# Kernel optimization log

Measured on AMD Instinct MI355X. Metric: run time of the kernel, lower is better.

The kernel has to match this reference:

```python
import jax, jax.numpy as jnp
import numpy as np

N_NODES = 50000

def gcn_conv(x, src, dst, ew, W, b):
    # PyG GCNConv: transform first, then D^-1/2 (A+I) D^-1/2 aggregation.
    h = x @ W                                   # [N, F_out]
    deg = jnp.zeros((N_NODES,), x.dtype).at[dst].add(ew)
    dis = jnp.where(deg > 0, jax.lax.rsqrt(deg), 0.0)
    norm = dis[src] * ew * dis[dst]             # [E]
    msg = norm[:, None] * h[src]                # [E, F_out]
    out = jax.ops.segment_sum(msg, dst, num_segments=N_NODES)
    return out + b

def setup_inputs() -> dict:
    key = jax.random.key(0)
    ks = jax.random.split(key, 9)
    x = jax.random.normal(ks[0], (N_NODES, 512), jnp.float32)
    edge_index = jax.random.randint(ks[1], (2, 800000), 0, N_NODES, jnp.int64)
    edge_attr = jax.random.uniform(ks[2], (800000,), jnp.float32)
    s = lambda f: 1.0 / np.sqrt(f)
    W1 = jax.random.normal(ks[3], (512, 64), jnp.float32) * s(512)
    b1 = jnp.zeros((64,), jnp.float32)
    W2 = jax.random.normal(ks[4], (64, 64), jnp.float32) * s(64)
    b2 = jnp.zeros((64,), jnp.float32)
    W3 = jax.random.normal(ks[5], (128, 128), jnp.float32) * s(128)
    b3 = jnp.zeros((128,), jnp.float32)
    return {"x": x, "edge_index": edge_index, "edge_attr": edge_attr,
            "W1": W1, "b1": b1, "W2": W2, "b2": b2, "W3": W3, "b3": b3}

def reference(x, edge_index, edge_attr, W1, b1, W2, b2, W3, b3):
    # add self-loops with weight 1 (GCNConv default)
    loops = jnp.arange(N_NODES, dtype=edge_index.dtype)
    src = jnp.concatenate([edge_index[0], loops])
    dst = jnp.concatenate([edge_index[1], loops])
    ew = jnp.concatenate([edge_attr, jnp.ones((N_NODES,), edge_attr.dtype)])
    h1 = gcn_conv(x, src, dst, ew, W1, b1)          # dropout is identity at eval
    h2 = gcn_conv(h1, src, dst, ew, W2, b2)
    h3 = gcn_conv(jnp.concatenate([h1, h2], axis=-1), src, dst, ew, W3, b3)
    return jax.nn.softmax(h3, axis=-1)
```

## Files before the change

### kernel.cpp

```cpp
#include <hip/hip_runtime.h>
#include <cstdint>
#include <cstddef>

#define NN 50000

typedef __attribute__((ext_vector_type(8))) short short8;
typedef __attribute__((ext_vector_type(4))) float f32x4;

__device__ inline ushort bf16_rne(float x) {
  uint u = __float_as_uint(x);
  uint r = u + 0x7FFFu + ((u >> 16) & 1u);
  return (ushort)(r >> 16);
}
__device__ inline float bf16_to_f(ushort h) { return __uint_as_float(((uint)h) << 16); }


#define NB2 256

__global__ __launch_bounds__(256) void k_hist(const int* __restrict__ dst,
                                              ushort* __restrict__ histmat, int E) {
  __shared__ uint lcnt[NN / 2];
  for (int i = threadIdx.x; i < NN / 2; i += 256) lcnt[i] = 0;
  __syncthreads();
  const int b = blockIdx.x;
  const int e0 = (int)((long long)E * b / NB2);
  const int e1 = (int)((long long)E * (b + 1) / NB2);
  for (int e = e0 + threadIdx.x; e < e1; e += 256) {
    int d = dst[e];
    atomicAdd(&lcnt[d >> 1], 1u << ((d & 1) * 16));
  }
  __syncthreads();
  uint* out = (uint*)(histmat + (size_t)b * NN);
  for (int i = threadIdx.x; i < NN / 2; i += 256) out[i] = lcnt[i];
}

__global__ __launch_bounds__(256) void k_colscan(ushort* __restrict__ histmat,
                                                 int* __restrict__ cnt, int N) {
  int n = blockIdx.x * 256 + threadIdx.x;
  if (n >= N) return;
  int run = 0;
  ushort* p = histmat + n;
#pragma unroll 8
  for (int b = 0; b < NB2; ++b) {
    int t = p[(size_t)b * NN];
    p[(size_t)b * NN] = (ushort)run;
    run += t;
  }
  cnt[n] = run;
}

__global__ __launch_bounds__(256) void k_scatter(const int* __restrict__ src,
                                                 const int* __restrict__ dst,
                                                 const float* __restrict__ ew,
                                                 const int* __restrict__ row_ptr,
                                                 const ushort* __restrict__ histmat,
                                                 int2* __restrict__ edge_s, int E) {
  __shared__ uint lcur[NN / 2];
  for (int i = threadIdx.x; i < NN / 2; i += 256) lcur[i] = 0;
  __syncthreads();
  const int b = blockIdx.x;
  const ushort* hb = histmat + (size_t)b * NN;
  const int e0 = (int)((long long)E * b / NB2);
  const int e1 = (int)((long long)E * (b + 1) / NB2);
  for (int e = e0 + threadIdx.x; e < e1; e += 256) {
    int d = dst[e];
    int sh = (d & 1) * 16;
    uint old = atomicAdd(&lcur[d >> 1], 1u << sh);
    int c = (int)((old >> sh) & 0xffffu);
    int pos = row_ptr[d] + (int)hb[d] + c;
    edge_s[pos] = make_int2(src[e], __float_as_int(ew[e]));
  }
}

__global__ __launch_bounds__(256) void k_degsum(const int* __restrict__ row_ptr,
                                                const int2* __restrict__ edge_s,
                                                float* __restrict__ dis, int N) {
  int n = blockIdx.x * 256 + threadIdx.x;
  if (n >= N) return;
  float sum = 1.0f;
  int e1 = row_ptr[n + 1];
  for (int p = row_ptr[n]; p < e1; ++p) sum += __int_as_float(edge_s[p].y);
  dis[n] = rsqrtf(sum);
}

__global__ __launch_bounds__(256) void k_wfix(int2* __restrict__ edge_s,
                                              const float* __restrict__ dis, int E) {
  int p = blockIdx.x * 256 + threadIdx.x;
  if (p >= E) return;
  int2 v = edge_s[p];
  edge_s[p] = make_int2(v.x, __float_as_int(dis[v.x] * __int_as_float(v.y)));
}


__global__ __launch_bounds__(256) void k_scan1(const int* __restrict__ in,
                                               int* __restrict__ out,
                                               int* __restrict__ bsum, int n) {
  __shared__ int ts[256];
  int base = blockIdx.x * 1024 + threadIdx.x * 4;
  int v[4] = {0, 0, 0, 0};
#pragma unroll
  for (int j = 0; j < 4; ++j) { int i = base + j; if (i < n) v[j] = in[i]; }
  int s = v[0] + v[1] + v[2] + v[3];
  ts[threadIdx.x] = s;
  __syncthreads();
  for (int o = 1; o < 256; o <<= 1) {
    int t = (threadIdx.x >= o) ? ts[threadIdx.x - o] : 0;
    __syncthreads();
    ts[threadIdx.x] += t;
    __syncthreads();
  }
  int run = ts[threadIdx.x] - s;
#pragma unroll
  for (int j = 0; j < 4; ++j) { int i = base + j; if (i < n) out[i] = run; run += v[j]; }
  if (threadIdx.x == 255) bsum[blockIdx.x] = ts[255];
}

__global__ void k_scan2(int* __restrict__ bsum, int nb, int* __restrict__ rpN, int E) {
  if (threadIdx.x == 0) {
    int run = 0;
    for (int b = 0; b < nb; ++b) { int t = bsum[b]; bsum[b] = run; run += t; }
    *rpN = E;
  }
}

__global__ __launch_bounds__(256) void k_scan3(int* __restrict__ out,
                                               const int* __restrict__ bsum, int n) {
  int i = blockIdx.x * 256 + threadIdx.x;
  if (i < n) out[i] += bsum[i >> 10];
}


__global__ __launch_bounds__(256) void k_wsplit(const float* __restrict__ W, int logF,
                                                int K, ushort* __restrict__ th,
                                                ushort* __restrict__ tl, int total) {
  int idx = blockIdx.x * 256 + threadIdx.x;
  if (idx >= total) return;
  int k = idx >> logF;
  int n = idx & ((1 << logF) - 1);
  float w = W[idx];
  ushort h = bf16_rne(w);
  float lof = w - bf16_to_f(h);
  ushort l = bf16_rne(lof);
  th[(size_t)n * K + k] = h;
  tl[(size_t)n * K + k] = l;
}

__global__ __launch_bounds__(256) void k_wprep(const float* __restrict__ W2,
                                               const float* __restrict__ W3,
                                               const float* __restrict__ b2,
                                               ushort* __restrict__ wch,
                                               ushort* __restrict__ wcl,
                                               float* __restrict__ bc) {
  int idx = blockIdx.x * 256 + threadIdx.x;
  int k = idx >> 7, n = idx & 127;
  float v;
  if (k < 64) {
    v = W3[k * 128 + n];
  } else {
    v = 0.f;
    const float* w2r = W2 + (k - 64) * 64;
    for (int j = 0; j < 64; ++j) v += w2r[j] * W3[(64 + j) * 128 + n];
  }
  ushort h = bf16_rne(v);
  wch[(size_t)n * 128 + k] = h;
  wcl[(size_t)n * 128 + k] = bf16_rne(v - bf16_to_f(h));
  if (idx < 128) {
    float s = 0.f;
    for (int j = 0; j < 64; ++j) s += b2[j] * W3[(64 + j) * 128 + idx];
    bc[idx] = s;
  }
}


template <int BN>
__global__ __launch_bounds__(256) void k_gemm_mfma(const float* __restrict__ A, int lda,
                                                   const ushort* __restrict__ BTh,
                                                   const ushort* __restrict__ BTl,
                                                   float* __restrict__ C, int ldc,
                                                   int N, int K) {
  constexpr int WN = BN / 2;
  constexpr int NT = WN / 16;
  __shared__ __align__(16) ushort Ah[64 * 64];
  __shared__ __align__(16) ushort Al[64 * 64];
  __shared__ __align__(16) ushort Bh[BN * 64];
  __shared__ __align__(16) ushort Bl[BN * 64];

  const int tid = threadIdx.x;
  const int lane = tid & 63;
  const int wid = tid >> 6;
  const int wm = wid >> 1;
  const int wn = wid & 1;
  const int bm = blockIdx.x * 64;
  const int l15 = lane & 15;
  const int kgrp = (lane >> 4) << 4;

  f32x4 acc[2][NT] = {};

  for (int kt = 0; kt < K; kt += 64) {
#pragma unroll
    for (int p = 0; p < 4; ++p) {
      int s = tid + p * 256;
      int m = s >> 4;
      int k4 = (s & 15) << 2;
      int gr = bm + m;
      float4 v = make_float4(0.f, 0.f, 0.f, 0.f);
      if (gr < N) v = *(const float4*)(A + (size_t)gr * lda + kt + k4);
      ushort4 h, l;
      h.x = bf16_rne(v.x); l.x = bf16_rne(v.x - bf16_to_f(h.x));
      h.y = bf16_rne(v.y); l.y = bf16_rne(v.y - bf16_to_f(h.y));
      h.z = bf16_rne(v.z); l.z = bf16_rne(v.z - bf16_to_f(h.z));
      h.w = bf16_rne(v.w); l.w = bf16_rne(v.w - bf16_to_f(h.w));
      int byo = (m * 128 + (k4 << 1)) ^ ((m & 7) << 4);
      *(ushort4*)((char*)Ah + byo) = h;
      *(ushort4*)((char*)Al + byo) = l;
    }
#pragma unroll
    for (int it = 0; it < BN / 32; ++it) {
      int s = tid + it * 256;
      int n = s >> 3;
      int kc = (s & 7) << 3;
      float4 vh = *(const float4*)(BTh + (size_t)n * K + kt + kc);
      float4 vl = *(const float4*)(BTl + (size_t)n * K + kt + kc);
      int byo = (n * 128 + (kc << 1)) ^ ((n & 7) << 4);
      *(float4*)((char*)Bh + byo) = vh;
      *(float4*)((char*)Bl + byo) = vl;
    }
    __syncthreads();
#pragma unroll
    for (int ks = 0; ks < 2; ++ks) {
      int kb = ks * 64 + kgrp;
      short8 ah[2], al[2];
#pragma unroll
      for (int i = 0; i < 2; ++i) {
        int row = wm * 32 + i * 16 + l15;
        int off = (row * 128 + kb) ^ ((row & 7) << 4);
        ah[i] = *(const short8*)((const char*)Ah + off);
        al[i] = *(const short8*)((const char*)Al + off);
      }
#pragma unroll
      for (int j = 0; j < NT; ++j) {
        int nr = wn * WN + j * 16 + l15;
        int off = (nr * 128 + kb) ^ ((nr & 7) << 4);
        short8 bh = *(const short8*)((const char*)Bh + off);
        short8 bl = *(const short8*)((const char*)Bl + off);
#pragma unroll
        for (int i = 0; i < 2; ++i) {
          acc[i][j] = __builtin_amdgcn_mfma_f32_16x16x32_bf16(ah[i], bh, acc[i][j], 0, 0, 0);
          acc[i][j] = __builtin_amdgcn_mfma_f32_16x16x32_bf16(ah[i], bl, acc[i][j], 0, 0, 0);
          acc[i][j] = __builtin_amdgcn_mfma_f32_16x16x32_bf16(al[i], bh, acc[i][j], 0, 0, 0);
        }
      }
    }
    __syncthreads();
  }

  const int r4 = (lane >> 4) << 2;
#pragma unroll
  for (int i = 0; i < 2; ++i) {
    int rowb = bm + wm * 32 + i * 16 + r4;
#pragma unroll
    for (int j = 0; j < NT; ++j) {
      int col = wn * WN + j * 16 + l15;
#pragma unroll
      for (int q = 0; q < 4; ++q) {
        int row = rowb + q;
        if (row < N) C[(size_t)row * ldc + col] = acc[i][j][q];
      }
    }
  }
}


__global__ __launch_bounds__(256) void k_gemm_smax(const float* __restrict__ A1,
                                                   const float* __restrict__ A2,
                                                   const ushort* __restrict__ BTh,
                                                   const ushort* __restrict__ BTl,
                                                   float* __restrict__ Cout,
                                                   const float* __restrict__ c,
                                                   const float* __restrict__ bc,
                                                   const float* __restrict__ b3,
                                                   int N) {
  constexpr int WN = 64, NT = 4, K = 128;
  __shared__ __align__(16) ushort smem[24576];
  ushort* Ah = smem;
  ushort* Al = smem + 4096;
  ushort* Bh = smem + 8192;
  ushort* Bl = smem + 16384;

  const int tid = threadIdx.x;
  const int lane = tid & 63;
  const int wid = tid >> 6;
  const int wm = wid >> 1;
  const int wn = wid & 1;
  const int bm = blockIdx.x * 64;
  const int l15 = lane & 15;
  const int kgrp = (lane >> 4) << 4;

  f32x4 acc[2][NT] = {};

  for (int kt = 0; kt < K; kt += 64) {
    const float* Asrc = (kt == 0) ? A1 : A2;
#pragma unroll
    for (int p = 0; p < 4; ++p) {
      int s = tid + p * 256;
      int m = s >> 4;
      int k4 = (s & 15) << 2;
      int gr = bm + m;
      float4 v = make_float4(0.f, 0.f, 0.f, 0.f);
      if (gr < N) v = *(const float4*)(Asrc + (size_t)gr * 64 + k4);
      ushort4 h, l;
      h.x = bf16_rne(v.x); l.x = bf16_rne(v.x - bf16_to_f(h.x));
      h.y = bf16_rne(v.y); l.y = bf16_rne(v.y - bf16_to_f(h.y));
      h.z = bf16_rne(v.z); l.z = bf16_rne(v.z - bf16_to_f(h.z));
      h.w = bf16_rne(v.w); l.w = bf16_rne(v.w - bf16_to_f(h.w));
      int byo = (m * 128 + (k4 << 1)) ^ ((m & 7) << 4);
      *(ushort4*)((char*)Ah + byo) = h;
      *(ushort4*)((char*)Al + byo) = l;
    }
#pragma unroll
    for (int it = 0; it < 4; ++it) {
      int s = tid + it * 256;
      int n = s >> 3;
      int kc = (s & 7) << 3;
      float4 vh = *(const float4*)(BTh + (size_t)n * K + kt + kc);
      float4 vl = *(const float4*)(BTl + (size_t)n * K + kt + kc);
      int byo = (n * 128 + (kc << 1)) ^ ((n & 7) << 4);
      *(float4*)((char*)Bh + byo) = vh;
      *(float4*)((char*)Bl + byo) = vl;
    }
    __syncthreads();
#pragma unroll
    for (int ks = 0; ks < 2; ++ks) {
      int kb = ks * 64 + kgrp;
      short8 ah[2], al[2];
#pragma unroll
      for (int i = 0; i < 2; ++i) {
        int row = wm * 32 + i * 16 + l15;
        int off = (row * 128 + kb) ^ ((row & 7) << 4);
        ah[i] = *(const short8*)((const char*)Ah + off);
        al[i] = *(const short8*)((const char*)Al + off);
      }
#pragma unroll
      for (int j = 0; j < NT; ++j) {
        int nr = wn * WN + j * 16 + l15;
        int off = (nr * 128 + kb) ^ ((nr & 7) << 4);
        short8 bh = *(const short8*)((const char*)Bh + off);
        short8 bl = *(const short8*)((const char*)Bl + off);
#pragma unroll
        for (int i = 0; i < 2; ++i) {
          acc[i][j] = __builtin_amdgcn_mfma_f32_16x16x32_bf16(ah[i], bh, acc[i][j], 0, 0, 0);
          acc[i][j] = __builtin_amdgcn_mfma_f32_16x16x32_bf16(ah[i], bl, acc[i][j], 0, 0, 0);
          acc[i][j] = __builtin_amdgcn_mfma_f32_16x16x32_bf16(al[i], bh, acc[i][j], 0, 0, 0);
        }
      }
    }
    __syncthreads();
  }

  float* hs = (float*)smem;
  float* pm = hs + 64 * 129;
  float* ps = pm + 256;

  const int r4 = (lane >> 4) << 2;
#pragma unroll
  for (int i = 0; i < 2; ++i) {
#pragma unroll
    for (int j = 0; j < NT; ++j) {
      int colb = wn * WN + j * 16 + l15;
      float cbv = bc[colb];
      float b3v = b3[colb];
#pragma unroll
      for (int q = 0; q < 4; ++q) {
        int rl = wm * 32 + i * 16 + r4 + q;
        int grow = bm + rl;
        float cv = (grow < N) ? c[grow] : 0.f;
        hs[rl * 129 + colb] = acc[i][j][q] + cv * cbv + b3v;
      }
    }
  }
  __syncthreads();

  int row = tid >> 2;
  int cs = (tid & 3) * 32;
  float ev[32];
  float m = -3.4e38f;
#pragma unroll
  for (int k = 0; k < 32; ++k) { ev[k] = hs[row * 129 + cs + k]; m = fmaxf(m, ev[k]); }
  float s = 0.f;
#pragma unroll
  for (int k = 0; k < 32; ++k) { ev[k] = __expf(ev[k] - m); s += ev[k]; }
  pm[row * 4 + (tid & 3)] = m;
  ps[row * 4 + (tid & 3)] = s;
  __syncthreads();
  float m0 = pm[row * 4 + 0], m1 = pm[row * 4 + 1];
  float m2 = pm[row * 4 + 2], m3 = pm[row * 4 + 3];
  float M = fmaxf(fmaxf(m0, m1), fmaxf(m2, m3));
  float S = ps[row * 4 + 0] * __expf(m0 - M) + ps[row * 4 + 1] * __expf(m1 - M) +
            ps[row * 4 + 2] * __expf(m2 - M) + ps[row * 4 + 3] * __expf(m3 - M);
  float f = __expf(pm[row * 4 + (tid & 3)] - M) / S;
  int grow = bm + row;
  if (grow < N) {
    float4* op = (float4*)(Cout + (size_t)grow * 128 + cs);
#pragma unroll
    for (int k = 0; k < 32; k += 4)
      op[k >> 2] = make_float4(ev[k] * f, ev[k + 1] * f, ev[k + 2] * f, ev[k + 3] * f);
  }
}


template <int LOGF, bool CSUM>
__global__ __launch_bounds__(256) void k_gather8(const float* __restrict__ t, int ldt,
                                                 const int* __restrict__ row_ptr,
                                                 const int2* __restrict__ edge_s,
                                                 const float* __restrict__ dis,
                                                 const float* __restrict__ bias,
                                                 float* __restrict__ out, int ldo,
                                                 float* __restrict__ cvec, int N) {
  constexpr int F = 1 << LOGF;
  constexpr int TPN = F / 4;
  int node = blockIdx.x * (256 / TPN) + threadIdx.x / TPN;
  if (node >= N) return;
  int f4 = (threadIdx.x % TPN) * 4;

  float4 a0, a1, a2, a3;
  a0.x = a0.y = a0.z = a0.w = 0.f;
  a1.x = a1.y = a1.z = a1.w = 0.f;
  a2.x = a2.y = a2.z = a2.w = 0.f;
  a3.x = a3.y = a3.z = a3.w = 0.f;
  float sw = 0.f;

  const int beg = row_ptr[node], end = row_ptr[node + 1];
  int i = beg;
  for (; i + 8 <= end; i += 8) {
    int2 e0 = edge_s[i], e1 = edge_s[i + 1], e2 = edge_s[i + 2], e3 = edge_s[i + 3];
    int2 e4 = edge_s[i + 4], e5 = edge_s[i + 5], e6 = edge_s[i + 6], e7 = edge_s[i + 7];
    float4 v0 = *(const float4*)(t + (size_t)e0.x * ldt + f4);
    float4 v1 = *(const float4*)(t + (size_t)e1.x * ldt + f4);
    float4 v2 = *(const float4*)(t + (size_t)e2.x * ldt + f4);
    float4 v3 = *(const float4*)(t + (size_t)e3.x * ldt + f4);
    float4 v4 = *(const float4*)(t + (size_t)e4.x * ldt + f4);
    float4 v5 = *(const float4*)(t + (size_t)e5.x * ldt + f4);
    float4 v6 = *(const float4*)(t + (size_t)e6.x * ldt + f4);
    float4 v7 = *(const float4*)(t + (size_t)e7.x * ldt + f4);
    float w0 = __int_as_float(e0.y), w1 = __int_as_float(e1.y);
    float w2 = __int_as_float(e2.y), w3 = __int_as_float(e3.y);
    float w4 = __int_as_float(e4.y), w5 = __int_as_float(e5.y);
    float w6 = __int_as_float(e6.y), w7 = __int_as_float(e7.y);
    if (CSUM) sw += (w0 + w1) + (w2 + w3) + (w4 + w5) + (w6 + w7);
    a0.x += w0 * v0.x; a0.y += w0 * v0.y; a0.z += w0 * v0.z; a0.w += w0 * v0.w;
    a1.x += w1 * v1.x; a1.y += w1 * v1.y; a1.z += w1 * v1.z; a1.w += w1 * v1.w;
    a2.x += w2 * v2.x; a2.y += w2 * v2.y; a2.z += w2 * v2.z; a2.w += w2 * v2.w;
    a3.x += w3 * v3.x; a3.y += w3 * v3.y; a3.z += w3 * v3.z; a3.w += w3 * v3.w;
    a0.x += w4 * v4.x; a0.y += w4 * v4.y; a0.z += w4 * v4.z; a0.w += w4 * v4.w;
    a1.x += w5 * v5.x; a1.y += w5 * v5.y; a1.z += w5 * v5.z; a1.w += w5 * v5.w;
    a2.x += w6 * v6.x; a2.y += w6 * v6.y; a2.z += w6 * v6.z; a2.w += w6 * v6.w;
    a3.x += w7 * v7.x; a3.y += w7 * v7.y; a3.z += w7 * v7.z; a3.w += w7 * v7.w;
  }
  for (; i < end; ++i) {
    int2 e0 = edge_s[i];
    float w0 = __int_as_float(e0.y);
    if (CSUM) sw += w0;
    float4 v0 = *(const float4*)(t + (size_t)e0.x * ldt + f4);
    a0.x += w0 * v0.x; a0.y += w0 * v0.y; a0.z += w0 * v0.z; a0.w += w0 * v0.w;
  }

  const float dn = dis[node];
  const float dd = dn * dn;
  const float4 tv = *(const float4*)(t + (size_t)node * ldt + f4);
  float4 bv = make_float4(0.f, 0.f, 0.f, 0.f);
  if (bias) bv = *(const float4*)(bias + f4);
  float4 v;
  v.x = bv.x + dd * tv.x + dn * (a0.x + a1.x + a2.x + a3.x);
  v.y = bv.y + dd * tv.y + dn * (a0.y + a1.y + a2.y + a3.y);
  v.z = bv.z + dd * tv.z + dn * (a0.z + a1.z + a2.z + a3.z);
  v.w = bv.w + dd * tv.w + dn * (a0.w + a1.w + a2.w + a3.w);
  *(float4*)(out + (size_t)node * ldo + f4) = v;
  if (CSUM && (threadIdx.x % TPN) == 0) cvec[node] = dn * (dn + sw);
}


__global__ __launch_bounds__(256) void k_gemm(const float* __restrict__ A, int lda,
                                              const float* __restrict__ B, int ldb,
                                              float* __restrict__ C, int ldc,
                                              int N, int K) {
  __shared__ float As[64][68];
  __shared__ float Bs[64][68];
  const int tid = threadIdx.x;
  const int bm = blockIdx.x * 64;
  const int bn = blockIdx.y * 64;
  const int tx = tid & 15;
  const int ty = tid >> 4;
  float acc[4][4] = {};
  for (int kt = 0; kt < K; kt += 64) {
#pragma unroll
    for (int p = 0; p < 4; ++p) {
      int s = tid + p * 256;
      int r = s >> 4;
      int c4 = (s & 15) << 2;
      float4 va = make_float4(0.f, 0.f, 0.f, 0.f);
      int gr = bm + r;
      if (gr < N) va = *(const float4*)(A + (size_t)gr * lda + kt + c4);
      As[c4 + 0][r] = va.x; As[c4 + 1][r] = va.y;
      As[c4 + 2][r] = va.z; As[c4 + 3][r] = va.w;
      float4 vb = *(const float4*)(B + (size_t)(kt + r) * ldb + bn + c4);
      *(float4*)(&Bs[r][c4]) = vb;
    }
    __syncthreads();
#pragma unroll
    for (int kk = 0; kk < 64; ++kk) {
      float4 a4 = *(const float4*)(&As[kk][ty * 4]);
      float4 b4 = *(const float4*)(&Bs[kk][tx * 4]);
      float a[4] = {a4.x, a4.y, a4.z, a4.w};
      float b[4] = {b4.x, b4.y, b4.z, b4.w};
#pragma unroll
      for (int i = 0; i < 4; ++i)
#pragma unroll
        for (int j = 0; j < 4; ++j) acc[i][j] += a[i] * b[j];
    }
    __syncthreads();
  }
#pragma unroll
  for (int i = 0; i < 4; ++i) {
    int gr = bm + ty * 4 + i;
    if (gr < N) {
      float4 v = make_float4(acc[i][0], acc[i][1], acc[i][2], acc[i][3]);
      *(float4*)(C + (size_t)gr * ldc + bn + tx * 4) = v;
    }
  }
}

__global__ __launch_bounds__(256) void k_deg_only(const int* __restrict__ dst,
                                                  const float* __restrict__ ew,
                                                  float* __restrict__ deg, int E) {
  int e = blockIdx.x * 256 + threadIdx.x;
  if (e < E) atomicAdd(&deg[dst[e]], ew[e]);
}

__global__ __launch_bounds__(256) void k_set1(float* __restrict__ p, int n) {
  int i = blockIdx.x * 256 + threadIdx.x;
  if (i < n) p[i] = 1.0f;
}

__global__ __launch_bounds__(256) void k_rsqrt(float* __restrict__ p, int n) {
  int i = blockIdx.x * 256 + threadIdx.x;
  if (i < n) p[i] = rsqrtf(p[i]);
}

__global__ __launch_bounds__(256) void k_norm(const int* __restrict__ src,
                                              const int* __restrict__ dst,
                                              const float* __restrict__ ew,
                                              const float* __restrict__ dis,
                                              float* __restrict__ nrm, int E) {
  int e = blockIdx.x * 256 + threadIdx.x;
  if (e < E) nrm[e] = dis[src[e]] * ew[e] * dis[dst[e]];
}

template <int LOGF>
__global__ __launch_bounds__(256) void k_agg_init(const float* __restrict__ t,
                                                  const float* __restrict__ dis,
                                                  const float* __restrict__ bias,
                                                  float* __restrict__ out, int ldo,
                                                  int coloff, int n_total) {
  int idx = blockIdx.x * 256 + threadIdx.x;
  if (idx >= n_total) return;
  int n = idx >> LOGF;
  int f = idx & ((1 << LOGF) - 1);
  float d = dis[n];
  out[(size_t)n * ldo + coloff + f] = bias[f] + d * d * t[idx];
}

template <int LOGF>
__global__ __launch_bounds__(256) void k_agg_edges(const float* __restrict__ t,
                                                   const int* __restrict__ src,
                                                   const int* __restrict__ dst,
                                                   const float* __restrict__ nrm,
                                                   float* __restrict__ out, int ldo,
                                                   int coloff, int E) {
  constexpr int F = 1 << LOGF;
  constexpr int EPB = 256 >> LOGF;
  int e = blockIdx.x * EPB + (threadIdx.x >> LOGF);
  if (e >= E) return;
  int f = threadIdx.x & (F - 1);
  int s = src[e];
  int d = dst[e];
  float v = nrm[e] * t[(size_t)s * F + f];
  atomicAdd(&out[(size_t)d * ldo + coloff + f], v);
}

__global__ __launch_bounds__(256) void k_softmax128(float* __restrict__ h, int N) {
  int row = blockIdx.x * 4 + (threadIdx.x >> 6);
  if (row >= N) return;
  int lane = threadIdx.x & 63;
  float* p = h + (size_t)row * 128;
  float v0 = p[lane];
  float v1 = p[lane + 64];
  float m = fmaxf(v0, v1);
#pragma unroll
  for (int o = 32; o > 0; o >>= 1) m = fmaxf(m, __shfl_xor(m, o));
  float e0 = __expf(v0 - m);
  float e1 = __expf(v1 - m);
  float sum = e0 + e1;
#pragma unroll
  for (int o = 32; o > 0; o >>= 1) sum += __shfl_xor(sum, o);
  float inv = 1.0f / sum;
  p[lane] = e0 * inv;
  p[lane + 64] = e1 * inv;
}

extern "C" void kernel_launch(void* const* d_in, const int* in_sizes, int n_in,
                              void* d_out, int out_size, void* d_ws, size_t ws_size,
                              hipStream_t stream) {
  const float* x = (const float*)d_in[0];
  const int* ei = (const int*)d_in[1];
  const float* ea = (const float*)d_in[2];
  const float* W1 = (const float*)d_in[3];
  const float* b1 = (const float*)d_in[4];
  const float* W2 = (const float*)d_in[5];
  const float* b2 = (const float*)d_in[6];
  const float* W3 = (const float*)d_in[7];
  const float* b3 = (const float*)d_in[8];

  const int N = NN;
  const int E = in_sizes[2];
  const int* src = ei;
  const int* dst = ei + E;

  char* ws = (char*)d_ws;
  size_t off = 0;
  auto alloc = [&](size_t bytes) {
    void* p = (void*)(ws + off);
    off += (bytes + 255) & ~(size_t)255;
    return p;
  };

  float* dis = (float*)alloc((size_t)N * 4);
  int* row_ptr = (int*)alloc((size_t)(N + 1) * 4);
  int* cnt = (int*)alloc((size_t)N * 4);
  int* bsum = (int*)alloc(256 * 4);
  float* cvec = (float*)alloc((size_t)N * 4);
  int2* edge_s = (int2*)alloc((size_t)E * 8);
  float* t12 = (float*)alloc((size_t)N * 128 * 4);
  float* H = (float*)alloc((size_t)N * 128 * 4);
  ushort* wch = (ushort*)alloc(128 * 128 * 2);
  ushort* wcl = (ushort*)alloc(128 * 128 * 2);
  ushort* w1h = (ushort*)alloc((size_t)512 * 64 * 2);
  ushort* w1l = (ushort*)alloc((size_t)512 * 64 * 2);
  float* bcv = (float*)alloc(128 * 4);
  size_t need_sort = off;
  float* out = (float*)d_out;
  float* bufA = t12;
  float* bufB = t12 + (size_t)N * 64;
  ushort* histmat = (ushort*)H;

  const bool useSort = (ws_size >= need_sort);
  const int NB_SCAN = (N + 1023) / 1024;
  const int GM = (N + 63) / 64;

  if (useSort) {
    k_wsplit<<<(512 * 64 + 255) / 256, 256, 0, stream>>>(W1, 6, 512, w1h, w1l, 512 * 64);
    k_wprep<<<64, 256, 0, stream>>>(W2, W3, b2, wch, wcl, bcv);

    k_hist<<<NB2, 256, 0, stream>>>(dst, histmat, E);
    k_colscan<<<(N + 255) / 256, 256, 0, stream>>>(histmat, cnt, N);
    k_scan1<<<NB_SCAN, 256, 0, stream>>>(cnt, row_ptr, bsum, N);
    k_scan2<<<1, 64, 0, stream>>>(bsum, NB_SCAN, row_ptr + N, E);
    k_scan3<<<(N + 255) / 256, 256, 0, stream>>>(row_ptr, bsum, N);
    k_scatter<<<NB2, 256, 0, stream>>>(src, dst, ea, row_ptr, histmat, edge_s, E);
    k_degsum<<<(N + 255) / 256, 256, 0, stream>>>(row_ptr, edge_s, dis, N);
    k_wfix<<<(E + 255) / 256, 256, 0, stream>>>(edge_s, dis, E);

    k_gemm_mfma<64><<<GM, 256, 0, stream>>>(x, 512, w1h, w1l, bufA, 64, N, 512);
    k_gather8<6, true><<<(N + 15) / 16, 256, 0, stream>>>(bufA, 64, row_ptr, edge_s,
                                                          dis, b1, bufB, 64, cvec, N);
    k_gather8<6, false><<<(N + 15) / 16, 256, 0, stream>>>(bufB, 64, row_ptr, edge_s,
                                                           dis, nullptr, bufA, 64,
                                                           nullptr, N);
    k_gather8<6, false><<<(N + 15) / 16, 256, 0, stream>>>(bufA, 64, row_ptr, edge_s,
                                                           dis, nullptr, bufB, 64,
                                                           nullptr, N);
    k_gemm_smax<<<GM, 256, 0, stream>>>(bufA, bufB, wch, wcl, out, cvec, bcv, b3, N);
  } else {
    off = 0;
    dis = (float*)alloc((size_t)N * 4);
    float* nrm = (float*)alloc((size_t)E * 4);
    t12 = (float*)alloc((size_t)N * 128 * 4);
    H = (float*)alloc((size_t)N * 128 * 4);
    const int tot64 = N * 64, tot128 = N * 128;
    dim3 g64(GM, 1), g128(GM, 2);

    k_set1<<<(N + 255) / 256, 256, 0, stream>>>(dis, N);
    k_deg_only<<<(E + 255) / 256, 256, 0, stream>>>(dst, ea, dis, E);
    k_rsqrt<<<(N + 255) / 256, 256, 0, stream>>>(dis, N);
    k_norm<<<(E + 255) / 256, 256, 0, stream>>>(src, dst, ea, dis, nrm, E);

    k_gemm<<<g64, 256, 0, stream>>>(x, 512, W1, 64, t12, 64, N, 512);
    k_agg_init<6><<<(tot64 + 255) / 256, 256, 0, stream>>>(t12, dis, b1, H, 128, 0, tot64);
    k_agg_edges<6><<<(E + 3) / 4, 256, 0, stream>>>(t12, src, dst, nrm, H, 128, 0, E);

    k_gemm<<<g64, 256, 0, stream>>>(H, 128, W2, 64, t12, 64, N, 64);
    k_agg_init<6><<<(tot64 + 255) / 256, 256, 0, stream>>>(t12, dis, b2, H, 128, 64, tot64);
    k_agg_edges<6><<<(E + 3) / 4, 256, 0, stream>>>(t12, src, dst, nrm, H, 128, 64, E);

    k_gemm<<<g128, 256, 0, stream>>>(H, 128, W3, 128, t12, 128, N, 128);
    k_agg_init<7><<<(tot128 + 255) / 256, 256, 0, stream>>>(t12, dis, b3, out, 128, 0, tot128);
    k_agg_edges<7><<<(E + 1) / 2, 256, 0, stream>>>(t12, src, dst, nrm, out, 128, 0, E);

    k_softmax128<<<(N + 3) / 4, 256, 0, stream>>>(out, N);
  }
}
```

Before: 239.0 us.

## Fuse weight prep kernels, fold edge-weight fix into first gather, enlarge GEMM1 tile

Merges the two weight-preparation kernels into one launch. Removes the separate edge-weight normalization pass by having the first gather multiply weights by dis[src] and write them back for later gathers. Replaces the templated MFMA GEMM with a 128-row, 512-thread specialization for the first layer, and halves the number of histogram/scatter blocks. The fused write-back adds extra scattered stores and dis lookups inside the first gather, and the smaller block count reduces parallelism in hist/scatter.

Result: no change. 238.2 us (-0.3%).

```diff
diff --git a/kernel.cpp b/kernel.cpp
--- a/kernel.cpp
+++ b/kernel.cpp
@@ -15,7 +15,7 @@
 __device__ inline float bf16_to_f(ushort h) { return __uint_as_float(((uint)h) << 16); }
 
 
-#define NB2 256
+#define NB2 128
 
 __global__ __launch_bounds__(256) void k_hist(const int* __restrict__ dst,
                                               ushort* __restrict__ histmat, int E) {
@@ -83,14 +83,6 @@
   dis[n] = rsqrtf(sum);
 }
 
-__global__ __launch_bounds__(256) void k_wfix(int2* __restrict__ edge_s,
-                                              const float* __restrict__ dis, int E) {
-  int p = blockIdx.x * 256 + threadIdx.x;
-  if (p >= E) return;
-  int2 v = edge_s[p];
-  edge_s[p] = make_int2(v.x, __float_as_int(dis[v.x] * __int_as_float(v.y)));
-}
-
 
 __global__ __launch_bounds__(256) void k_scan1(const int* __restrict__ in,
                                                int* __restrict__ out,
@@ -130,81 +122,76 @@
 }
 
 
-__global__ __launch_bounds__(256) void k_wsplit(const float* __restrict__ W, int logF,
-                                                int K, ushort* __restrict__ th,
-                                                ushort* __restrict__ tl, int total) {
-  int idx = blockIdx.x * 256 + threadIdx.x;
-  if (idx >= total) return;
-  int k = idx >> logF;
-  int n = idx & ((1 << logF) - 1);
-  float w = W[idx];
-  ushort h = bf16_rne(w);
-  float lof = w - bf16_to_f(h);
-  ushort l = bf16_rne(lof);
-  th[(size_t)n * K + k] = h;
-  tl[(size_t)n * K + k] = l;
-}
-
-__global__ __launch_bounds__(256) void k_wprep(const float* __restrict__ W2,
-                                               const float* __restrict__ W3,
-                                               const float* __restrict__ b2,
-                                               ushort* __restrict__ wch,
-                                               ushort* __restrict__ wcl,
-                                               float* __restrict__ bc) {
-  int idx = blockIdx.x * 256 + threadIdx.x;
-  int k = idx >> 7, n = idx & 127;
-  float v;
-  if (k < 64) {
-    v = W3[k * 128 + n];
+__global__ __launch_bounds__(256) void k_wprep_all(const float* __restrict__ W1,
+                                                   const float* __restrict__ W2,
+                                                   const float* __restrict__ W3,
+                                                   const float* __restrict__ b2,
+                                                   ushort* __restrict__ w1h,
+                                                   ushort* __restrict__ w1l,
+                                                   ushort* __restrict__ wch,
+                                                   ushort* __restrict__ wcl,
+                                                   float* __restrict__ bc) {
+  int b = blockIdx.x;
+  if (b < 128) {
+    int idx = b * 256 + threadIdx.x;
+    int k = idx >> 6, n = idx & 63;
+    float w = W1[idx];
+    ushort h = bf16_rne(w);
+    w1h[(size_t)n * 512 + k] = h;
+    w1l[(size_t)n * 512 + k] = bf16_rne(w - bf16_to_f(h));
   } else {
-    v = 0.f;
-    const float* w2r = W2 + (k - 64) * 64;
-    for (int j = 0; j < 64; ++j) v += w2r[j] * W3[(64 + j) * 128 + n];
-  }
-  ushort h = bf16_rne(v);
-  wch[(size_t)n * 128 + k] = h;
-  wcl[(size_t)n * 128 + k] = bf16_rne(v - bf16_to_f(h));
-  if (idx < 128) {
-    float s = 0.f;
-    for (int j = 0; j < 64; ++j) s += b2[j] * W3[(64 + j) * 128 + idx];
-    bc[idx] = s;
-  }
-}
-
-
-template <int BN>
-__global__ __launch_bounds__(256) void k_gemm_mfma(const float* __restrict__ A, int lda,
-                                                   const ushort* __restrict__ BTh,
-                                                   const ushort* __restrict__ BTl,
-                                                   float* __restrict__ C, int ldc,
-                                                   int N, int K) {
-  constexpr int WN = BN / 2;
-  constexpr int NT = WN / 16;
-  __shared__ __align__(16) ushort Ah[64 * 64];
-  __shared__ __align__(16) ushort Al[64 * 64];
-  __shared__ __align__(16) ushort Bh[BN * 64];
-  __shared__ __align__(16) ushort Bl[BN * 64];
+    int idx = (b - 128) * 256 + threadIdx.x;
+    int k = idx >> 7, n = idx & 127;
+    float v;
+    if (k < 64) {
+      v = W3[k * 128 + n];
+    } else {
+      v = 0.f;
+      const float* w2r = W2 + (k - 64) * 64;
+      for (int j = 0; j < 64; ++j) v += w2r[j] * W3[(64 + j) * 128 + n];
+    }
+    ushort h = bf16_rne(v);
+    wch[(size_t)n * 128 + k] = h;
+    wcl[(size_t)n * 128 + k] = bf16_rne(v - bf16_to_f(h));
+    if (idx < 128) {
+      float s = 0.f;
+      for (int j = 0; j < 64; ++j) s += b2[j] * W3[(64 + j) * 128 + idx];
+      bc[idx] = s;
+    }
+  }
+}
+
+
+__global__ __launch_bounds__(512) void k_gemm1(const float* __restrict__ A,
+                                               const ushort* __restrict__ BTh,
+                                               const ushort* __restrict__ BTl,
+                                               float* __restrict__ C, int N) {
+  constexpr int K = 512;
+  __shared__ __align__(16) ushort Ah[128 * 64];
+  __shared__ __align__(16) ushort Al[128 * 64];
+  __shared__ __align__(16) ushort Bh[64 * 64];
+  __shared__ __align__(16) ushort Bl[64 * 64];
 
   const int tid = threadIdx.x;
   const int lane = tid & 63;
   const int wid = tid >> 6;
   const int wm = wid >> 1;
   const int wn = wid & 1;
-  const int bm = blockIdx.x * 64;
+  const int bm = blockIdx.x * 128;
   const int l15 = lane & 15;
   const int kgrp = (lane >> 4) << 4;
 
-  f32x4 acc[2][NT] = {};
+  f32x4 acc[2][2] = {};
 
   for (int kt = 0; kt < K; kt += 64) {
 #pragma unroll
     for (int p = 0; p < 4; ++p) {
-      int s = tid + p * 256;
+      int s = tid + p * 512;
       int m = s >> 4;
       int k4 = (s & 15) << 2;
       int gr = bm + m;
       float4 v = make_float4(0.f, 0.f, 0.f, 0.f);
-      if (gr < N) v = *(const float4*)(A + (size_t)gr * lda + kt + k4);
+      if (gr < N) v = *(const float4*)(A + (size_t)gr * K + kt + k4);
       ushort4 h, l;
       h.x = bf16_rne(v.x); l.x = bf16_rne(v.x - bf16_to_f(h.x));
       h.y = bf16_rne(v.y); l.y = bf16_rne(v.y - bf16_to_f(h.y));
@@ -214,9 +201,8 @@
       *(ushort4*)((char*)Ah + byo) = h;
       *(ushort4*)((char*)Al + byo) = l;
     }
-#pragma unroll
-    for (int it = 0; it < BN / 32; ++it) {
-      int s = tid + it * 256;
+    {
+      int s = tid;
       int n = s >> 3;
       int kc = (s & 7) << 3;
       float4 vh = *(const float4*)(BTh + (size_t)n * K + kt + kc);
@@ -238,8 +224,8 @@
         al[i] = *(const short8*)((const char*)Al + off);
       }
 #pragma unroll
-      for (int j = 0; j < NT; ++j) {
-        int nr = wn * WN + j * 16 + l15;
+      for (int j = 0; j < 2; ++j) {
+        int nr = wn * 32 + j * 16 + l15;
         int off = (nr * 128 + kb) ^ ((nr & 7) << 4);
         short8 bh = *(const short8*)((const char*)Bh + off);
         short8 bl = *(const short8*)((const char*)Bl + off);
@@ -257,14 +243,13 @@
   const int r4 = (lane >> 4) << 2;
 #pragma unroll
   for (int i = 0; i < 2; ++i) {
-    int rowb = bm + wm * 32 + i * 16 + r4;
-#pragma unroll
-    for (int j = 0; j < NT; ++j) {
-      int col = wn * WN + j * 16 + l15;
+#pragma unroll
+    for (int j = 0; j < 2; ++j) {
+      int col = wn * 32 + j * 16 + l15;
 #pragma unroll
       for (int q = 0; q < 4; ++q) {
-        int row = rowb + q;
-        if (row < N) C[(size_t)row * ldc + col] = acc[i][j][q];
+        int row = bm + wm * 32 + i * 16 + r4 + q;
+        if (row < N) C[(size_t)row * 64 + col] = acc[i][j][q];
       }
     }
   }
@@ -408,10 +393,10 @@
 }
 
 
-template <int LOGF, bool CSUM>
+template <int LOGF, bool CSUM, bool WFIX>
 __global__ __launch_bounds__(256) void k_gather8(const float* __restrict__ t, int ldt,
                                                  const int* __restrict__ row_ptr,
-                                                 const int2* __restrict__ edge_s,
+                                                 int2* __restrict__ edge_s,
                                                  const float* __restrict__ dis,
                                                  const float* __restrict__ bias,
                                                  float* __restrict__ out, int ldo,
@@ -421,6 +406,7 @@
   int node = blockIdx.x * (256 / TPN) + threadIdx.x / TPN;
   if (node >= N) return;
   int f4 = (threadIdx.x % TPN) * 4;
+  const bool lead = (threadIdx.x % TPN) == 0;
 
   float4 a0, a1, a2, a3;
   a0.x = a0.y = a0.z = a0.w = 0.f;
@@ -446,6 +432,16 @@
     float w2 = __int_as_float(e2.y), w3 = __int_as_float(e3.y);
     float w4 = __int_as_float(e4.y), w5 = __int_as_float(e5.y);
     float w6 = __int_as_float(e6.y), w7 = __int_as_float(e7.y);
+    if (WFIX) {
+      w0 *= dis[e0.x]; w1 *= dis[e1.x]; w2 *= dis[e2.x]; w3 *= dis[e3.x];
+      w4 *= dis[e4.x]; w5 *= dis[e5.x]; w6 *= dis[e6.x]; w7 *= dis[e7.x];
+      if (lead) {
+        edge_s[i].y = __float_as_int(w0);     edge_s[i + 1].y = __float_as_int(w1);
+        edge_s[i + 2].y = __float_as_int(w2); edge_s[i + 3].y = __float_as_int(w3);
+        edge_s[i + 4].y = __float_as_int(w4); edge_s[i + 5].y = __float_as_int(w5);
+        edge_s[i + 6].y = __float_as_int(w6); edge_s[i + 7].y = __float_as_int(w7);
+      }
+    }
     if (CSUM) sw += (w0 + w1) + (w2 + w3) + (w4 + w5) + (w6 + w7);
     a0.x += w0 * v0.x; a0.y += w0 * v0.y; a0.z += w0 * v0.z; a0.w += w0 * v0.w;
     a1.x += w1 * v1.x; a1.y += w1 * v1.y; a1.z += w1 * v1.z; a1.w += w1 * v1.w;
@@ -459,6 +455,10 @@
   for (; i < end; ++i) {
     int2 e0 = edge_s[i];
     float w0 = __int_as_float(e0.y);
+    if (WFIX) {
+      w0 *= dis[e0.x];
+      if (lead) edge_s[i].y = __float_as_int(w0);
+    }
     if (CSUM) sw += w0;
     float4 v0 = *(const float4*)(t + (size_t)e0.x * ldt + f4);
     a0.x += w0 * v0.x; a0.y += w0 * v0.y; a0.z += w0 * v0.z; a0.w += w0 * v0.w;
@@ -475,7 +475,7 @@
   v.z = bv.z + dd * tv.z + dn * (a0.z + a1.z + a2.z + a3.z);
   v.w = bv.w + dd * tv.w + dn * (a0.w + a1.w + a2.w + a3.w);
   *(float4*)(out + (size_t)node * ldo + f4) = v;
-  if (CSUM && (threadIdx.x % TPN) == 0) cvec[node] = dn * (dn + sw);
+  if (CSUM && lead) cvec[node] = dn * (dn + sw);
 }
 
 
@@ -657,8 +657,7 @@
   const int GM = (N + 63) / 64;
 
   if (useSort) {
-    k_wsplit<<<(512 * 64 + 255) / 256, 256, 0, stream>>>(W1, 6, 512, w1h, w1l, 512 * 64);
-    k_wprep<<<64, 256, 0, stream>>>(W2, W3, b2, wch, wcl, bcv);
+    k_wprep_all<<<192, 256, 0, stream>>>(W1, W2, W3, b2, w1h, w1l, wch, wcl, bcv);
 
     k_hist<<<NB2, 256, 0, stream>>>(dst, histmat, E);
     k_colscan<<<(N + 255) / 256, 256, 0, stream>>>(histmat, cnt, N);
@@ -667,17 +666,14 @@
     k_scan3<<<(N + 255) / 256, 256, 0, stream>>>(row_ptr, bsum, N);
     k_scatter<<<NB2, 256, 0, stream>>>(src, dst, ea, row_ptr, histmat, edge_s, E);
     k_degsum<<<(N + 255) / 256, 256, 0, stream>>>(row_ptr, edge_s, dis, N);
-    k_wfix<<<(E + 255) / 256, 256, 0, stream>>>(edge_s, dis, E);
-
-    k_gemm_mfma<64><<<GM, 256, 0, stream>>>(x, 512, w1h, w1l, bufA, 64, N, 512);
-    k_gather8<6, true><<<(N + 15) / 16, 256, 0, stream>>>(bufA, 64, row_ptr, edge_s,
-                                                          dis, b1, bufB, 64, cvec, N);
-    k_gather8<6, false><<<(N + 15) / 16, 256, 0, stream>>>(bufB, 64, row_ptr, edge_s,
-                                                           dis, nullptr, bufA, 64,
-                                                           nullptr, N);
-    k_gather8<6, false><<<(N + 15) / 16, 256, 0, stream>>>(bufA, 64, row_ptr, edge_s,
-                                                           dis, nullptr, bufB, 64,
-                                                           nullptr, N);
+
+    k_gemm1<<<(N + 127) / 128, 512, 0, stream>>>(x, w1h, w1l, bufA, N);
+    k_gather8<6, true, true><<<(N + 15) / 16, 256, 0, stream>>>(
+        bufA, 64, row_ptr, edge_s, dis, b1, bufB, 64, cvec, N);
+    k_gather8<6, false, false><<<(N + 15) / 16, 256, 0, stream>>>(
+        bufB, 64, row_ptr, edge_s, dis, nullptr, bufA, 64, nullptr, N);
+    k_gather8<6, false, false><<<(N + 15) / 16, 256, 0, stream>>>(
+        bufA, 64, row_ptr, edge_s, dis, nullptr, bufB, 64, nullptr, N);
     k_gemm_smax<<<GM, 256, 0, stream>>>(bufA, bufB, wch, wcl, out, cvec, bcv, b3, N);
   } else {
     off = 0;
```
